# Kernel tuning notes

Hardware: AMD Instinct MI355X
Metric: run time of the kernel (lower is better)

Reference implementation:

```python
import jax, jax.numpy as jnp
import numpy as np

B, HEADS, SCALES, POINTS, HIDDEN = 1, 8, 4, 4, 192
HEAD_DIM = HIDDEN // HEADS
OFFSET_SCALE = 0.35
EPS = 1e-5


def conv1x1(x, W, b=None):
    # x: [B,C,D,H,W], W: [O,C]
    y = jnp.einsum('bcdhw,oc->bodhw', x, W)
    if b is not None:
        y = y + b[None, :, None, None, None]
    return y


def base_grid(D, H, W, dtype):
    z = jnp.linspace(-1.0, 1.0, D, dtype=dtype)
    y = jnp.linspace(-1.0, 1.0, H, dtype=dtype)
    x = jnp.linspace(-1.0, 1.0, W, dtype=dtype)
    zz, yy, xx = jnp.meshgrid(z, y, x, indexing='ij')
    return jnp.stack((xx, yy, zz), axis=-1)  # [D,H,W,3] (x,y,z order)


def trilinear_sample(val, grid):
    # val: [BH,C,Dv,Hv,Wv]; grid: [BH,N,3] normalized (x,y,z), align_corners=False, border padding
    BH, C, Dv, Hv, Wv = val.shape
    unnorm = lambda g, s: jnp.clip(((g + 1.0) * s - 1.0) * 0.5, 0.0, s - 1.0)
    ix = unnorm(grid[..., 0], Wv)
    iy = unnorm(grid[..., 1], Hv)
    iz = unnorm(grid[..., 2], Dv)
    x0f, y0f, z0f = jnp.floor(ix), jnp.floor(iy), jnp.floor(iz)
    wx, wy, wz = ix - x0f, iy - y0f, iz - z0f
    x0 = x0f.astype(jnp.int32); x1 = jnp.minimum(x0 + 1, Wv - 1)
    y0 = y0f.astype(jnp.int32); y1 = jnp.minimum(y0 + 1, Hv - 1)
    z0 = z0f.astype(jnp.int32); z1 = jnp.minimum(z0 + 1, Dv - 1)
    vflat = val.reshape(BH, C, Dv * Hv * Wv)
    gather = jax.vmap(lambda v, i: v[:, i])  # -> [BH,C,N]
    def corner(zi, yi, xi):
        return gather(vflat, (zi * Hv + yi) * Wv + xi)
    w = lambda a: a[:, None, :]  # broadcast weight over channel dim
    out = (corner(z0, y0, x0) * w((1 - wz) * (1 - wy) * (1 - wx))
           + corner(z0, y0, x1) * w((1 - wz) * (1 - wy) * wx)
           + corner(z0, y1, x0) * w((1 - wz) * wy * (1 - wx))
           + corner(z0, y1, x1) * w((1 - wz) * wy * wx)
           + corner(z1, y0, x0) * w(wz * (1 - wy) * (1 - wx))
           + corner(z1, y0, x1) * w(wz * (1 - wy) * wx)
           + corner(z1, y1, x0) * w(wz * wy * (1 - wx))
           + corner(z1, y1, x1) * w(wz * wy * wx))
    return out


def fsad_forward(query_feature, values, Wq, Wvs, Woff, boff, Wwt, bwt, Wout, gamma, beta):
    Bq, _, D, H, W = query_feature.shape
    N = D * H * W
    q = conv1x1(query_feature, Wq)
    off = conv1x1(q, Woff, boff).reshape(Bq, HEADS, SCALES, POINTS, 3, D, H, W)
    off = jnp.tanh(off) * OFFSET_SCALE
    aw = conv1x1(q, Wwt, bwt).reshape(Bq, HEADS, SCALES * POINTS, D, H, W)
    aw = jax.nn.softmax(aw, axis=2).reshape(Bq, HEADS, SCALES, POINTS, D, H, W)
    bg = base_grid(D, H, W, q.dtype)  # [D,H,W,3]
    acc = jnp.zeros((Bq, HEADS, HEAD_DIM, D, H, W), q.dtype)
    for s in range(SCALES):
        feat = values[s]
        val = conv1x1(feat, Wvs[s]).reshape(Bq * HEADS, HEAD_DIM, *feat.shape[2:])
        # off[:,:,s]: [B,Hh,P,3,D,H,W] -> grid [B,Hh,P,D,H,W,3]
        grid = bg[None, None, None] + jnp.moveaxis(off[:, :, s], 3, -1)
        grid = grid.reshape(Bq * HEADS, POINTS * N, 3)
        sampled = trilinear_sample(val, grid).reshape(Bq, HEADS, HEAD_DIM, POINTS, D, H, W)
        acc = acc + jnp.einsum('bhcpdyx,bhpdyx->bhcdyx', sampled, aw[:, :, s])
    out = conv1x1(acc.reshape(Bq, HIDDEN, D, H, W), Wout)
    # InstanceNorm3d(affine=True)
    mu = out.mean(axis=(2, 3, 4), keepdims=True)
    var = out.var(axis=(2, 3, 4), keepdims=True)
    out = (out - mu) * jax.lax.rsqrt(var + EPS)
    return out * gamma[None, :, None, None, None] + beta[None, :, None, None, None]


def setup_inputs() -> dict:
    key = jax.random.key(0)
    ks = jax.random.split(key, 16)
    value_channels = [32, 64, 128, 256]
    sizes = [64, 32, 16, 8]
    inp = {
        'query_feature': jax.random.normal(ks[0], (1, 128, 16, 16, 16), jnp.float32),
        'v0': jax.random.normal(ks[1], (1, 32, 64, 64, 64), jnp.float32),
        'v1': jax.random.normal(ks[2], (1, 64, 32, 32, 32), jnp.float32),
        'v2': jax.random.normal(ks[3], (1, 128, 16, 16, 16), jnp.float32),
        'v3': jax.random.normal(ks[4], (1, 256, 8, 8, 8), jnp.float32),
        'Wq': jax.random.normal(ks[5], (HIDDEN, 128), jnp.float32) * 0.05,
        'Wv0': jax.random.normal(ks[6], (HIDDEN, 32), jnp.float32) * 0.05,
        'Wv1': jax.random.normal(ks[7], (HIDDEN, 64), jnp.float32) * 0.05,
        'Wv2': jax.random.normal(ks[8], (HIDDEN, 128), jnp.float32) * 0.05,
        'Wv3': jax.random.normal(ks[9], (HIDDEN, 256), jnp.float32) * 0.05,
        'Woff': jax.random.normal(ks[10], (HEADS * SCALES * POINTS * 3, HIDDEN), jnp.float32) * 0.05,
        'boff': jnp.zeros((HEADS * SCALES * POINTS * 3,), jnp.float32),
        'Wwt': jax.random.normal(ks[11], (HEADS * SCALES * POINTS, HIDDEN), jnp.float32) * 0.05,
        'bwt': jnp.zeros((HEADS * SCALES * POINTS,), jnp.float32),
        'Wout': jax.random.normal(ks[12], (128, HIDDEN), jnp.float32) * 0.05,
        'gamma': jnp.ones((128,), jnp.float32),
        'beta': jnp.zeros((128,), jnp.float32),
    }
    return inp


def reference(query_feature, v0, v1, v2, v3, Wq, Wv0, Wv1, Wv2, Wv3, Woff, boff, Wwt, bwt, Wout, gamma, beta):
    return fsad_forward(query_feature, [v0, v1, v2, v3], Wq, [Wv0, Wv1, Wv2, Wv3], Woff, boff, Wwt, bwt, Wout, gamma, beta)
```

## Files before the change

### kernel.cpp

```cpp
#include <hip/hip_runtime.h>
#include <hip/hip_fp16.h>
#include <cmath>

#define N_Q 4096
#define HEADS 8
#define HEAD_DIM 24
#define HIDDEN 192

__device__ __forceinline__ float4 ld4(const float* p) { return *(const float4*)p; }

__device__ __forceinline__ void fma8h(float* u, float w, const __half* p) {
    uint4 raw = *(const uint4*)p;
    const __half2* h2 = reinterpret_cast<const __half2*>(&raw);
#pragma unroll
    for (int k = 0; k < 4; k++) {
        float2 f = __half22float2(h2[k]);
        u[2 * k]     = fmaf(w, f.x, u[2 * k]);
        u[2 * k + 1] = fmaf(w, f.y, u[2 * k + 1]);
    }
}

__device__ __forceinline__ void corner24(float* acc, float w, const __half* p) {
    fma8h(acc,      w, p);
    fma8h(acc + 8,  w, p + 8);
    fma8h(acc + 16, w, p + 16);
}

__global__ __launch_bounds__(256)
void wcomb_kernel(const float* __restrict__ Woff, const float* __restrict__ Wwt,
                  const float* __restrict__ Wq, const float* __restrict__ boff,
                  const float* __restrict__ bwt, float* __restrict__ Wcomb,
                  float* __restrict__ biasc)
{
    int o = blockIdx.x * 2 + (threadIdx.x >> 7);
    int c = threadIdx.x & 127;
    const float* A = (o < 384) ? (Woff + (size_t)o * 192) : (Wwt + (size_t)(o - 384) * 192);
    float s = 0.f;
#pragma unroll 4
    for (int k = 0; k < 192; k++) s = fmaf(A[k], Wq[k * 128 + c], s);
    Wcomb[(size_t)o * 128 + c] = s;
    if (c == 0) biasc[o] = (o < 384) ? boff[o] : bwt[o - 384];
}

template<int C, int OG, int MODE>
__global__ __launch_bounds__(256)
void convT_kernel(const float* __restrict__ W, const float* __restrict__ bias,
                  const float* __restrict__ x, float* __restrict__ y)
{
    __shared__ float xs[C * 64];
    __shared__ float Wl[OG * C];
    int tid = threadIdx.x;
    int n0 = blockIdx.x * 64;
    int og0 = blockIdx.y * OG;
    for (int k = tid; k < C * 64; k += 256) xs[k] = x[(size_t)(k >> 6) * N_Q + n0 + (k & 63)];
    for (int k = tid; k < OG * C; k += 256) Wl[k] = W[(size_t)(og0 + k / C) * C + (k % C)];
    __syncthreads();

    int wv = tid >> 6, lane = tid & 63;
    constexpr int PT = OG / 4;
    float acc[PT];
#pragma unroll
    for (int i = 0; i < PT; i++) acc[i] = 0.f;
    for (int c = 0; c < C; c++) {
        float xv = xs[c * 64 + lane];
#pragma unroll
        for (int i = 0; i < PT; i++)
            acc[i] = fmaf(Wl[(wv * PT + i) * C + c], xv, acc[i]);
    }
#pragma unroll
    for (int i = 0; i < PT; i++) {
        int o = og0 + wv * PT + i;
        float r = acc[i];
        if constexpr (MODE == 3) {
            r = (o < 384) ? tanhf(r + bias[o]) * 0.35f : r + bias[o];
        }
        y[(size_t)o * N_Q + n0 + lane] = r;
    }
}

__global__ __launch_bounds__(256)
void softmax16_kernel(float* __restrict__ aw)
{
    int idx = blockIdx.x * 256 + threadIdx.x;
    int h = idx >> 12;
    int n = idx & 4095;
    float v[16];
    float m = -1e30f;
#pragma unroll
    for (int i = 0; i < 16; i++) { v[i] = aw[(h * 16 + i) * N_Q + n]; m = fmaxf(m, v[i]); }
    float ssum = 0.f;
#pragma unroll
    for (int i = 0; i < 16; i++) { v[i] = __expf(v[i] - m); ssum += v[i]; }
    float inv = 1.0f / ssum;
#pragma unroll
    for (int i = 0; i < 16; i++) aw[(h * 16 + i) * N_Q + n] = v[i] * inv;
}

template<int C, int P>
__global__ __launch_bounds__(256)
void transpose_h_kernel(const float* __restrict__ src, __half* __restrict__ dst, int Nv)
{
    __shared__ float lds[P][C + 1];
    int tid = threadIdx.x;
    int pos0 = blockIdx.x * P;
    for (int k = tid; k < P * C; k += 256) {
        int c = k / P, p = k % P;
        lds[p][c] = src[c * Nv + pos0 + p];
    }
    __syncthreads();
    for (int k = tid; k < P * C; k += 256) {
        int p = k / C, c = k % C;
        dst[(pos0 + p) * C + c] = __float2half(lds[p][c]);
    }
}

template<int C, int OG>
__device__ __forceinline__ void valconv_body(const float* __restrict__ Wv,
                                             const float* __restrict__ v,
                                             __half* __restrict__ valT, int Nv,
                                             int bx, int by, int tid)
{
    __shared__ float Wl[OG][C];
    __shared__ __half outs[64 * OG];
    int p0 = bx * 64;
    int og0 = by * OG;
    for (int k = tid; k < OG * C; k += 256) Wl[k / C][k % C] = Wv[(size_t)(og0 + k / C) * C + (k % C)];
    __syncthreads();

    int osub = tid >> 6;
    int lane = tid & 63;
    constexpr int PT = OG / 4;
    float acc[PT];
#pragma unroll
    for (int i = 0; i < PT; i++) acc[i] = 0.f;
    for (int c = 0; c < C; c++) {
        float vv = v[(size_t)c * Nv + p0 + lane];
#pragma unroll
        for (int i = 0; i < PT; i++)
            acc[i] = fmaf(Wl[osub * PT + i][c], vv, acc[i]);
    }
#pragma unroll
    for (int i = 0; i < PT; i++)
        outs[lane * OG + osub * PT + i] = __float2half(acc[i]);
    __syncthreads();

    unsigned int* dst = (unsigned int*)valT;
    const unsigned int* src = (const unsigned int*)outs;
    constexpr int UPP = OG / 2;
    for (int k = tid; k < 64 * UPP; k += 256) {
        int p = k / UPP, i = k % UPP;
        dst[(size_t)(p0 + p) * (HIDDEN / 2) + (og0 / 2) + i] = src[p * UPP + i];
    }
}

__global__ __launch_bounds__(256)
void valconv_all_kernel(const float* __restrict__ Wv1, const float* __restrict__ v1,
                        __half* __restrict__ val1T,
                        const float* __restrict__ Wv2, const float* __restrict__ v2,
                        __half* __restrict__ val2T,
                        const float* __restrict__ Wv3, const float* __restrict__ v3,
                        __half* __restrict__ val3T)
{
    int id = blockIdx.x;
    int tid = threadIdx.x;
    if (id < 4096) {
        valconv_body<64, 24>(Wv1, v1, val1T, 32768, id & 511, id >> 9, tid);
    } else if (id < 5120) {
        int i2 = id - 4096;
        valconv_body<128, 12>(Wv2, v2, val2T, 4096, i2 & 63, i2 >> 6, tid);
    } else {
        int i3 = id - 5120;
        valconv_body<256, 8>(Wv3, v3, val3T, 512, i3 & 7, i3 >> 3, tid);
    }
}

__global__ __launch_bounds__(256)
void sample_kernel(const float* __restrict__ offb, const float* __restrict__ awb,
                   const __half* __restrict__ v0T, const __half* __restrict__ val1T,
                   const __half* __restrict__ val2T, const __half* __restrict__ val3T,
                   const float* __restrict__ Wv0,
                   __half* __restrict__ accb)
{
    int tid = threadIdx.x;
    int id = blockIdx.x;
    int t = id & 15;
    int h = (id >> 4) & 7;
    int sp = id >> 7;
    int n = t * 256 + tid;
    int s = sp >> 2, p = sp & 3;

    int wx = n & 15, hy = (n >> 4) & 15, dz = n >> 8;
    const float step = 2.0f / 15.0f;
    float bx = -1.f + wx * step;
    float by = -1.f + hy * step;
    float bz = -1.f + dz * step;

    float acc[HEAD_DIM];
#pragma unroll
    for (int j = 0; j < HEAD_DIM; j++) acc[j] = 0.f;

    int S = 64;
    const __half* srcT = v0T;
    if (s == 1)      { S = 32; srcT = val1T; }
    else if (s == 2) { S = 16; srcT = val2T; }
    else if (s == 3) { S = 8;  srcT = val3T; }
    float fS = (float)S;

    int orow = ((h * 4 + s) * 4 + p) * 3;
    float ox = offb[(orow + 0) * N_Q + n];
    float oy = offb[(orow + 1) * N_Q + n];
    float oz = offb[(orow + 2) * N_Q + n];
    float awv = awb[(h * 16 + s * 4 + p) * N_Q + n];

    float ix = fminf(fmaxf(((bx + ox + 1.f) * fS - 1.f) * 0.5f, 0.f), fS - 1.f);
    float iy = fminf(fmaxf(((by + oy + 1.f) * fS - 1.f) * 0.5f, 0.f), fS - 1.f);
    float iz = fminf(fmaxf(((bz + oz + 1.f) * fS - 1.f) * 0.5f, 0.f), fS - 1.f);

    float x0f = floorf(ix), y0f = floorf(iy), z0f = floorf(iz);
    float fx = ix - x0f, fy = iy - y0f, fz = iz - z0f;
    int x0 = (int)x0f, y0 = (int)y0f, z0 = (int)z0f;
    int x1 = min(x0 + 1, S - 1), y1 = min(y0 + 1, S - 1), z1 = min(z0 + 1, S - 1);

    int r000 = (z0 * S + y0) * S + x0, r001 = (z0 * S + y0) * S + x1;
    int r010 = (z0 * S + y1) * S + x0, r011 = (z0 * S + y1) * S + x1;
    int r100 = (z1 * S + y0) * S + x0, r101 = (z1 * S + y0) * S + x1;
    int r110 = (z1 * S + y1) * S + x0, r111 = (z1 * S + y1) * S + x1;

    float gx1 = fx, gx0 = 1.f - fx;
    float gy1 = fy, gy0 = 1.f - fy;
    float gz1 = fz, gz0 = 1.f - fz;
    float w000 = gz0 * gy0 * gx0 * awv, w001 = gz0 * gy0 * gx1 * awv;
    float w010 = gz0 * gy1 * gx0 * awv, w011 = gz0 * gy1 * gx1 * awv;
    float w100 = gz1 * gy0 * gx0 * awv, w101 = gz1 * gy0 * gx1 * awv;
    float w110 = gz1 * gy1 * gx0 * awv, w111 = gz1 * gy1 * gx1 * awv;

    if (s == 0) {
        const float* Wvh = Wv0 + h * HEAD_DIM * 32;
#pragma unroll
        for (int c8 = 0; c8 < 32; c8 += 8) {
            float u[8] = {0.f, 0.f, 0.f, 0.f, 0.f, 0.f, 0.f, 0.f};
            fma8h(u, w000, srcT + r000 * 32 + c8);
            fma8h(u, w001, srcT + r001 * 32 + c8);
            fma8h(u, w010, srcT + r010 * 32 + c8);
            fma8h(u, w011, srcT + r011 * 32 + c8);
            fma8h(u, w100, srcT + r100 * 32 + c8);
            fma8h(u, w101, srcT + r101 * 32 + c8);
            fma8h(u, w110, srcT + r110 * 32 + c8);
            fma8h(u, w111, srcT + r111 * 32 + c8);
#pragma unroll
            for (int j = 0; j < HEAD_DIM; j++) {
                const float* wp = Wvh + j * 32 + c8;
                float4 wa = ld4(wp), wb = ld4(wp + 4);
                acc[j] = fmaf(wa.x, u[0], fmaf(wa.y, u[1], fmaf(wa.z, u[2], fmaf(wa.w, u[3],
                         fmaf(wb.x, u[4], fmaf(wb.y, u[5], fmaf(wb.z, u[6], fmaf(wb.w, u[7], acc[j]))))))));
            }
        }
    } else {
        const __half* base = srcT + h * HEAD_DIM;
        corner24(acc, w000, base + (size_t)r000 * HIDDEN);
        corner24(acc, w001, base + (size_t)r001 * HIDDEN);
        corner24(acc, w010, base + (size_t)r010 * HIDDEN);
        corner24(acc, w011, base + (size_t)r011 * HIDDEN);
        corner24(acc, w100, base + (size_t)r100 * HIDDEN);
        corner24(acc, w101, base + (size_t)r101 * HIDDEN);
        corner24(acc, w110, base + (size_t)r110 * HIDDEN);
        corner24(acc, w111, base + (size_t)r111 * HIDDEN);
    }

    __half* ab = accb + (size_t)sp * HIDDEN * N_Q;
#pragma unroll
    for (int j = 0; j < HEAD_DIM; j++) ab[(h * HEAD_DIM + j) * N_Q + n] = __float2half(acc[j]);
}

__global__ __launch_bounds__(256)
void accsum_kernel(const __half* __restrict__ accb, float* __restrict__ accsum)
{
    int i = blockIdx.x * 256 + threadIdx.x;
    const int SB8 = HIDDEN * N_Q / 8;
    const uint4* src = (const uint4*)accb;
    float a[8] = {0.f, 0.f, 0.f, 0.f, 0.f, 0.f, 0.f, 0.f};
#pragma unroll
    for (int sp = 0; sp < 16; sp++) {
        uint4 r = src[sp * SB8 + i];
        const __half2* h2 = (const __half2*)&r;
#pragma unroll
        for (int k = 0; k < 4; k++) {
            float2 f = __half22float2(h2[k]);
            a[2 * k] += f.x; a[2 * k + 1] += f.y;
        }
    }
    float4* dst = (float4*)accsum;
    dst[i * 2]     = make_float4(a[0], a[1], a[2], a[3]);
    dst[i * 2 + 1] = make_float4(a[4], a[5], a[6], a[7]);
}

__global__ __launch_bounds__(256)
void inorm_kernel(float* __restrict__ out, const float* __restrict__ gamma,
                  const float* __restrict__ beta)
{
    int o = blockIdx.x;
    int tid = threadIdx.x;
    float s = 0.f, s2 = 0.f;
    for (int n = tid; n < N_Q; n += 256) {
        float v = out[o * N_Q + n];
        s += v; s2 += v * v;
    }
    __shared__ float rs[256], rs2[256];
    rs[tid] = s; rs2[tid] = s2;
    __syncthreads();
    for (int k = 128; k > 0; k >>= 1) {
        if (tid < k) { rs[tid] += rs[tid + k]; rs2[tid] += rs2[tid + k]; }
        __syncthreads();
    }
    float mu = rs[0] * (1.0f / N_Q);
    float var = rs2[0] * (1.0f / N_Q) - mu * mu;
    float rstd = rsqrtf(var + 1e-5f);
    float g = gamma[o] * rstd;
    float b = beta[o] - mu * g;
    for (int n = tid; n < N_Q; n += 256) {
        out[o * N_Q + n] = fmaf(out[o * N_Q + n], g, b);
    }
}

extern "C" void kernel_launch(void* const* d_in, const int* in_sizes, int n_in,
                              void* d_out, int out_size, void* d_ws, size_t ws_size,
                              hipStream_t stream)
{
    const float* qf    = (const float*)d_in[0];
    const float* v0    = (const float*)d_in[1];
    const float* v1    = (const float*)d_in[2];
    const float* v2    = (const float*)d_in[3];
    const float* v3    = (const float*)d_in[4];
    const float* Wq    = (const float*)d_in[5];
    const float* Wv0   = (const float*)d_in[6];
    const float* Wv1   = (const float*)d_in[7];
    const float* Wv2   = (const float*)d_in[8];
    const float* Wv3   = (const float*)d_in[9];
    const float* Woff  = (const float*)d_in[10];
    const float* boff  = (const float*)d_in[11];
    const float* Wwt   = (const float*)d_in[12];
    const float* bwt   = (const float*)d_in[13];
    const float* Wout  = (const float*)d_in[14];
    const float* gamma = (const float*)d_in[15];
    const float* beta  = (const float*)d_in[16];
    float* out = (float*)d_out;

    float* ws     = (float*)d_ws;
    float*  Wcomb  = ws;
    float*  biasc  = Wcomb  + 65536;
    float*  offb   = biasc  + 512;
    float*  awb    = offb   + 1572864;
    __half* v0T    = (__half*)(awb + 524288);
    __half* val1T  = (__half*)((float*)v0T + 4194304);
    __half* val2T  = (__half*)((float*)val1T + 3145728);
    __half* val3T  = (__half*)((float*)val2T + 393216);
    __half* accb   = (__half*)((float*)val3T + 49152);
    float*  accsum = (float*)accb + 6291456;

    wcomb_kernel<<<256, 256, 0, stream>>>(Woff, Wwt, Wq, boff, bwt, Wcomb, biasc);
    convT_kernel<128, 32, 3><<<dim3(64, 16), 256, 0, stream>>>(Wcomb, biasc, qf, offb);
    softmax16_kernel<<<128, 256, 0, stream>>>(awb);
    transpose_h_kernel<32, 256><<<1024, 256, 0, stream>>>(v0, v0T, 262144);
    valconv_all_kernel<<<5312, 256, 0, stream>>>(Wv1, v1, val1T, Wv2, v2, val2T, Wv3, v3, val3T);
    sample_kernel<<<2048, 256, 0, stream>>>(offb, awb, v0T, val1T, val2T, val3T, Wv0, accb);
    accsum_kernel<<<384, 256, 0, stream>>>(accb, accsum);
    convT_kernel<192, 32, 0><<<dim3(64, 4), 256, 0, stream>>>(Wout, nullptr, accsum, out);
    inorm_kernel<<<128, 256, 0, stream>>>(out, gamma, beta);
}
```

Before: 281.8 us.

## Merge prep kernels into one launch and fuse softmax into offset/weight conv

Combines the v0 transpose, the three value projections and the Wcomb weight fold into a single prep kernel that shares one static LDS buffer, dispatched by block index. The softmax over attention weights moves into the offset/weight projection kernel through an LDS staging tile, which removes a separate kernel and a round trip of the weight buffer through global memory. This cuts kernel launches and dependency gaps. The larger shared LDS allocation may lower occupancy for the lighter branches.

```diff
diff --git a/kernel.cpp b/kernel.cpp
--- a/kernel.cpp
+++ b/kernel.cpp
@@ -26,14 +26,74 @@
     fma8h(acc + 16, w, p + 16);
 }
 
-__global__ __launch_bounds__(256)
-void wcomb_kernel(const float* __restrict__ Woff, const float* __restrict__ Wwt,
-                  const float* __restrict__ Wq, const float* __restrict__ boff,
-                  const float* __restrict__ bwt, float* __restrict__ Wcomb,
-                  float* __restrict__ biasc)
-{
-    int o = blockIdx.x * 2 + (threadIdx.x >> 7);
-    int c = threadIdx.x & 127;
+
+__device__ __forceinline__ void transpose_body(char* smem, const float* __restrict__ src,
+                                               __half* __restrict__ dst, int bx, int tid)
+{
+    float (*lds)[33] = (float(*)[33])smem;
+    const int Nv = 262144;
+    int pos0 = bx * 256;
+    for (int k = tid; k < 256 * 32; k += 256) {
+        int c = k >> 8, p = k & 255;
+        lds[p][c] = src[(size_t)c * Nv + pos0 + p];
+    }
+    __syncthreads();
+    for (int k = tid; k < 256 * 32; k += 256) {
+        int p = k >> 5, c = k & 31;
+        dst[(size_t)(pos0 + p) * 32 + c] = __float2half(lds[p][c]);
+    }
+}
+
+template<int C, int OG>
+__device__ __forceinline__ void valconv_body(char* smem, const float* __restrict__ Wv,
+                                             const float* __restrict__ v,
+                                             __half* __restrict__ valT, int Nv,
+                                             int bx, int by, int tid)
+{
+    float* Wl = (float*)smem;
+    __half* outs = (__half*)(smem + OG * C * 4);
+    int p0 = bx * 64;
+    int og0 = by * OG;
+    for (int k = tid; k < OG * C; k += 256) Wl[k] = Wv[(size_t)(og0 + k / C) * C + (k % C)];
+    __syncthreads();
+
+    int osub = tid >> 6;
+    int lane = tid & 63;
+    constexpr int PT = OG / 4;
+    float acc[PT];
+#pragma unroll
+    for (int i = 0; i < PT; i++) acc[i] = 0.f;
+    for (int c = 0; c < C; c++) {
+        float vv = v[(size_t)c * Nv + p0 + lane];
+#pragma unroll
+        for (int i = 0; i < PT; i++)
+            acc[i] = fmaf(Wl[(osub * PT + i) * C + c], vv, acc[i]);
+    }
+#pragma unroll
+    for (int i = 0; i < PT; i++)
+        outs[lane * OG + osub * PT + i] = __float2half(acc[i]);
+    __syncthreads();
+
+    unsigned int* dst = (unsigned int*)valT;
+    const unsigned int* src = (const unsigned int*)outs;
+    constexpr int UPP = OG / 2;
+    for (int k = tid; k < 64 * UPP; k += 256) {
+        int p = k / UPP, i = k % UPP;
+        dst[(size_t)(p0 + p) * (HIDDEN / 2) + (og0 / 2) + i] = src[p * UPP + i];
+    }
+}
+
+__device__ __forceinline__ void wcomb_body(int bx, int tid,
+                                           const float* __restrict__ Woff,
+                                           const float* __restrict__ Wwt,
+                                           const float* __restrict__ Wq,
+                                           const float* __restrict__ boff,
+                                           const float* __restrict__ bwt,
+                                           float* __restrict__ Wcomb,
+                                           float* __restrict__ biasc)
+{
+    int o = bx * 2 + (tid >> 7);
+    int c = tid & 127;
     const float* A = (o < 384) ? (Woff + (size_t)o * 192) : (Wwt + (size_t)(o - 384) * 192);
     float s = 0.f;
 #pragma unroll 4
@@ -42,135 +102,89 @@
     if (c == 0) biasc[o] = (o < 384) ? boff[o] : bwt[o - 384];
 }
 
-template<int C, int OG, int MODE>
-__global__ __launch_bounds__(256)
-void convT_kernel(const float* __restrict__ W, const float* __restrict__ bias,
-                  const float* __restrict__ x, float* __restrict__ y)
-{
-    __shared__ float xs[C * 64];
-    __shared__ float Wl[OG * C];
+__global__ __launch_bounds__(256)
+void prep_kernel(const float* __restrict__ v0, __half* __restrict__ v0T,
+                 const float* __restrict__ Wv1, const float* __restrict__ v1, __half* __restrict__ val1T,
+                 const float* __restrict__ Wv2, const float* __restrict__ v2, __half* __restrict__ val2T,
+                 const float* __restrict__ Wv3, const float* __restrict__ v3, __half* __restrict__ val3T,
+                 const float* __restrict__ Woff, const float* __restrict__ Wwt,
+                 const float* __restrict__ Wq, const float* __restrict__ boff,
+                 const float* __restrict__ bwt, float* __restrict__ Wcomb,
+                 float* __restrict__ biasc)
+{
+    __shared__ __align__(16) char smem[33792];
+    int id = blockIdx.x;
+    int tid = threadIdx.x;
+    if (id < 1024) {
+        transpose_body(smem, v0, v0T, id, tid);
+    } else if (id < 5120) {
+        int i1 = id - 1024;
+        valconv_body<64, 24>(smem, Wv1, v1, val1T, 32768, i1 & 511, i1 >> 9, tid);
+    } else if (id < 6144) {
+        int i2 = id - 5120;
+        valconv_body<128, 12>(smem, Wv2, v2, val2T, 4096, i2 & 63, i2 >> 6, tid);
+    } else if (id < 6336) {
+        int i3 = id - 6144;
+        valconv_body<256, 8>(smem, Wv3, v3, val3T, 512, i3 & 7, i3 >> 3, tid);
+    } else {
+        wcomb_body(id - 6336, tid, Woff, Wwt, Wq, boff, bwt, Wcomb, biasc);
+    }
+}
+
+__global__ __launch_bounds__(256)
+void offaw_kernel(const float* __restrict__ Wcomb, const float* __restrict__ biasc,
+                  const float* __restrict__ qf, float* __restrict__ ob)
+{
+    __shared__ float xs[128 * 64];
+    __shared__ float Wl[32 * 128];
+    __shared__ float ls[32 * 64];
     int tid = threadIdx.x;
     int n0 = blockIdx.x * 64;
-    int og0 = blockIdx.y * OG;
-    for (int k = tid; k < C * 64; k += 256) xs[k] = x[(size_t)(k >> 6) * N_Q + n0 + (k & 63)];
-    for (int k = tid; k < OG * C; k += 256) Wl[k] = W[(size_t)(og0 + k / C) * C + (k % C)];
+    int og0 = blockIdx.y * 32;
+    for (int k = tid; k < 128 * 64; k += 256) xs[k] = qf[(size_t)(k >> 6) * N_Q + n0 + (k & 63)];
+    for (int k = tid; k < 32 * 128; k += 256) Wl[k] = Wcomb[(size_t)og0 * 128 + k];
     __syncthreads();
 
     int wv = tid >> 6, lane = tid & 63;
-    constexpr int PT = OG / 4;
-    float acc[PT];
-#pragma unroll
-    for (int i = 0; i < PT; i++) acc[i] = 0.f;
-    for (int c = 0; c < C; c++) {
+    float acc[8];
+#pragma unroll
+    for (int i = 0; i < 8; i++) acc[i] = 0.f;
+    for (int c = 0; c < 128; c++) {
         float xv = xs[c * 64 + lane];
 #pragma unroll
-        for (int i = 0; i < PT; i++)
-            acc[i] = fmaf(Wl[(wv * PT + i) * C + c], xv, acc[i]);
-    }
-#pragma unroll
-    for (int i = 0; i < PT; i++) {
-        int o = og0 + wv * PT + i;
-        float r = acc[i];
-        if constexpr (MODE == 3) {
-            r = (o < 384) ? tanhf(r + bias[o]) * 0.35f : r + bias[o];
+        for (int i = 0; i < 8; i++)
+            acc[i] = fmaf(Wl[(wv * 8 + i) * 128 + c], xv, acc[i]);
+    }
+
+    if (og0 < 384) {
+#pragma unroll
+        for (int i = 0; i < 8; i++) {
+            int o = og0 + wv * 8 + i;
+            ob[(size_t)o * N_Q + n0 + lane] = tanhf(acc[i] + biasc[o]) * 0.35f;
         }
-        y[(size_t)o * N_Q + n0 + lane] = r;
-    }
-}
-
-__global__ __launch_bounds__(256)
-void softmax16_kernel(float* __restrict__ aw)
-{
-    int idx = blockIdx.x * 256 + threadIdx.x;
-    int h = idx >> 12;
-    int n = idx & 4095;
-    float v[16];
-    float m = -1e30f;
-#pragma unroll
-    for (int i = 0; i < 16; i++) { v[i] = aw[(h * 16 + i) * N_Q + n]; m = fmaxf(m, v[i]); }
-    float ssum = 0.f;
-#pragma unroll
-    for (int i = 0; i < 16; i++) { v[i] = __expf(v[i] - m); ssum += v[i]; }
-    float inv = 1.0f / ssum;
-#pragma unroll
-    for (int i = 0; i < 16; i++) aw[(h * 16 + i) * N_Q + n] = v[i] * inv;
-}
-
-template<int C, int P>
-__global__ __launch_bounds__(256)
-void transpose_h_kernel(const float* __restrict__ src, __half* __restrict__ dst, int Nv)
-{
-    __shared__ float lds[P][C + 1];
-    int tid = threadIdx.x;
-    int pos0 = blockIdx.x * P;
-    for (int k = tid; k < P * C; k += 256) {
-        int c = k / P, p = k % P;
-        lds[p][c] = src[c * Nv + pos0 + p];
-    }
-    __syncthreads();
-    for (int k = tid; k < P * C; k += 256) {
-        int p = k / C, c = k % C;
-        dst[(pos0 + p) * C + c] = __float2half(lds[p][c]);
-    }
-}
-
-template<int C, int OG>
-__device__ __forceinline__ void valconv_body(const float* __restrict__ Wv,
-                                             const float* __restrict__ v,
-                                             __half* __restrict__ valT, int Nv,
-                                             int bx, int by, int tid)
-{
-    __shared__ float Wl[OG][C];
-    __shared__ __half outs[64 * OG];
-    int p0 = bx * 64;
-    int og0 = by * OG;
-    for (int k = tid; k < OG * C; k += 256) Wl[k / C][k % C] = Wv[(size_t)(og0 + k / C) * C + (k % C)];
-    __syncthreads();
-
-    int osub = tid >> 6;
-    int lane = tid & 63;
-    constexpr int PT = OG / 4;
-    float acc[PT];
-#pragma unroll
-    for (int i = 0; i < PT; i++) acc[i] = 0.f;
-    for (int c = 0; c < C; c++) {
-        float vv = v[(size_t)c * Nv + p0 + lane];
-#pragma unroll
-        for (int i = 0; i < PT; i++)
-            acc[i] = fmaf(Wl[osub * PT + i][c], vv, acc[i]);
-    }
-#pragma unroll
-    for (int i = 0; i < PT; i++)
-        outs[lane * OG + osub * PT + i] = __float2half(acc[i]);
-    __syncthreads();
-
-    unsigned int* dst = (unsigned int*)valT;
-    const unsigned int* src = (const unsigned int*)outs;
-    constexpr int UPP = OG / 2;
-    for (int k = tid; k < 64 * UPP; k += 256) {
-        int p = k / UPP, i = k % UPP;
-        dst[(size_t)(p0 + p) * (HIDDEN / 2) + (og0 / 2) + i] = src[p * UPP + i];
-    }
-}
-
-__global__ __launch_bounds__(256)
-void valconv_all_kernel(const float* __restrict__ Wv1, const float* __restrict__ v1,
-                        __half* __restrict__ val1T,
-                        const float* __restrict__ Wv2, const float* __restrict__ v2,
-                        __half* __restrict__ val2T,
-                        const float* __restrict__ Wv3, const float* __restrict__ v3,
-                        __half* __restrict__ val3T)
-{
-    int id = blockIdx.x;
-    int tid = threadIdx.x;
-    if (id < 4096) {
-        valconv_body<64, 24>(Wv1, v1, val1T, 32768, id & 511, id >> 9, tid);
-    } else if (id < 5120) {
-        int i2 = id - 4096;
-        valconv_body<128, 12>(Wv2, v2, val2T, 4096, i2 & 63, i2 >> 6, tid);
     } else {
-        int i3 = id - 5120;
-        valconv_body<256, 8>(Wv3, v3, val3T, 512, i3 & 7, i3 >> 3, tid);
+#pragma unroll
+        for (int i = 0; i < 8; i++) {
+            int o = og0 + wv * 8 + i;
+            ls[(wv * 8 + i) * 64 + lane] = acc[i] + biasc[o];
+        }
+        __syncthreads();
+        if (tid < 128) {
+            int hl = tid >> 6;
+            int n2 = tid & 63;
+            float v[16];
+            float m = -1e30f;
+#pragma unroll
+            for (int j = 0; j < 16; j++) { v[j] = ls[(hl * 16 + j) * 64 + n2]; m = fmaxf(m, v[j]); }
+            float ssum = 0.f;
+#pragma unroll
+            for (int j = 0; j < 16; j++) { v[j] = __expf(v[j] - m); ssum += v[j]; }
+            float inv = 1.0f / ssum;
+            int orow = og0 + hl * 16;
+#pragma unroll
+            for (int j = 0; j < 16; j++)
+                ob[(size_t)(orow + j) * N_Q + n0 + n2] = v[j] * inv;
+        }
     }
 }
 
@@ -292,6 +306,34 @@
     float4* dst = (float4*)accsum;
     dst[i * 2]     = make_float4(a[0], a[1], a[2], a[3]);
     dst[i * 2 + 1] = make_float4(a[4], a[5], a[6], a[7]);
+}
+
+__global__ __launch_bounds__(256)
+void outconv_kernel(const float* __restrict__ Wout, const float* __restrict__ accsum,
+                    float* __restrict__ out)
+{
+    __shared__ float xs[HIDDEN * 64];
+    __shared__ float Wl[32 * HIDDEN];
+    int tid = threadIdx.x;
+    int n0 = blockIdx.x * 64;
+    int og0 = blockIdx.y * 32;
+    for (int k = tid; k < HIDDEN * 64; k += 256) xs[k] = accsum[(size_t)(k >> 6) * N_Q + n0 + (k & 63)];
+    for (int k = tid; k < 32 * HIDDEN; k += 256) Wl[k] = Wout[(size_t)og0 * HIDDEN + k];
+    __syncthreads();
+
+    int wv = tid >> 6, lane = tid & 63;
+    float acc[8];
+#pragma unroll
+    for (int i = 0; i < 8; i++) acc[i] = 0.f;
+    for (int c = 0; c < HIDDEN; c++) {
+        float xv = xs[c * 64 + lane];
+#pragma unroll
+        for (int i = 0; i < 8; i++)
+            acc[i] = fmaf(Wl[(wv * 8 + i) * HIDDEN + c], xv, acc[i]);
+    }
+#pragma unroll
+    for (int i = 0; i < 8; i++)
+        out[(size_t)(og0 + wv * 8 + i) * N_Q + n0 + lane] = acc[i];
 }
 
 __global__ __launch_bounds__(256)
@@ -349,21 +391,20 @@
     float*  Wcomb  = ws;
     float*  biasc  = Wcomb  + 65536;
     float*  offb   = biasc  + 512;
-    float*  awb    = offb   + 1572864;
-    __half* v0T    = (__half*)(awb + 524288);
+    float*  awb    = offb   + 384 * 4096;
+    __half* v0T    = (__half*)(offb + 2097152);
     __half* val1T  = (__half*)((float*)v0T + 4194304);
     __half* val2T  = (__half*)((float*)val1T + 3145728);
     __half* val3T  = (__half*)((float*)val2T + 393216);
     __half* accb   = (__half*)((float*)val3T + 49152);
     float*  accsum = (float*)accb + 6291456;
 
-    wcomb_kernel<<<256, 256, 0, stream>>>(Woff, Wwt, Wq, boff, bwt, Wcomb, biasc);
-    convT_kernel<128, 32, 3><<<dim3(64, 16), 256, 0, stream>>>(Wcomb, biasc, qf, offb);
-    softmax16_kernel<<<128, 256, 0, stream>>>(awb);
-    transpose_h_kernel<32, 256><<<1024, 256, 0, stream>>>(v0, v0T, 262144);
-    valconv_all_kernel<<<5312, 256, 0, stream>>>(Wv1, v1, val1T, Wv2, v2, val2T, Wv3, v3, val3T);
+    prep_kernel<<<6592, 256, 0, stream>>>(v0, v0T, Wv1, v1, val1T, Wv2, v2, val2T,
+                                          Wv3, v3, val3T, Woff, Wwt, Wq, boff, bwt,
+                                          Wcomb, biasc);
+    offaw_kernel<<<dim3(64, 16), 256, 0, stream>>>(Wcomb, biasc, qf, offb);
     sample_kernel<<<2048, 256, 0, stream>>>(offb, awb, v0T, val1T, val2T, val3T, Wv0, accb);
     accsum_kernel<<<384, 256, 0, stream>>>(accb, accsum);
-    convT_kernel<192, 32, 0><<<dim3(64, 4), 256, 0, stream>>>(Wout, nullptr, accsum, out);
+    outconv_kernel<<<dim3(64, 4), 256, 0, stream>>>(Wout, accsum, out);
     inorm_kernel<<<128, 256, 0, stream>>>(out, gamma, beta);
 }
```

Measured after the change: 257.3 us. 1.09x faster.
